# Optimization experiments

Measured on AMD Instinct MI355X. Metric: run time of the kernel, lower is better.

The kernel has to match this reference:

```python
import jax, jax.numpy as jnp
import numpy as np

B, N, D = 16, 4096, 64
LB_TH = 0.01
L2_LAMDA = 0.001
RECONS_LAMDA = 0.2


def _xavier(key, shape):
    fan_in, fan_out = shape[0], shape[1]
    a = float(np.sqrt(6.0 / (fan_in + fan_out)))
    return jax.random.uniform(key, shape, jnp.float32, -a, a)


def setup_inputs() -> dict:
    key = jax.random.key(0)
    k1, k2, k3 = jax.random.split(key, 3)
    X = jax.random.normal(k1, (B, N, D), jnp.float32)
    r_proj = _xavier(k2, (D, D))
    incidence_m = _xavier(k3, (N, N - 1))
    return {"X": X, "r_proj": r_proj, "incidence_m": incidence_m}


def reference(X, r_proj, incidence_m):
    n = incidence_m.shape[0]
    # clamp(min=lb_th) followed by masked_fill(~(v > lb_th), 0) == keep only orig > lb_th
    w = jnp.where(incidence_m > LB_TH, incidence_m, jnp.zeros((), X.dtype))  # [N, N-1]
    # scatter each row's N-1 weights into an NxN matrix, skipping the diagonal
    rows = jnp.arange(n)[:, None]                      # [N,1]
    cols = jnp.arange(n - 1)[None, :]                  # [1,N-1]
    full_cols = cols + (cols >= rows).astype(cols.dtype)  # [N,N-1]
    W = jnp.zeros((n, n), X.dtype).at[rows, full_cols].set(w)
    # per-node projection of master node features: X @ r_proj
    X_proj = jnp.einsum('bnd,de->bne', X, r_proj)      # [B,N,D]
    # neighbor reconstruction for every node at once
    recon = jnp.einsum('ij,bjd->bid', W, X)            # [B,N,D]
    recon_err = jnp.sqrt(jnp.sum((X_proj - recon) ** 2, axis=-1))  # [B,N]
    l1 = jnp.max(jnp.abs(w), axis=1)                   # [N] (max over single-row sum == max abs)
    l2 = jnp.sqrt(jnp.sum(w ** 2, axis=1))             # [N]
    recon_loss = recon_err * RECONS_LAMDA + l1[None, :] + L2_LAMDA * l2[None, :]
    incidence_all = W + jnp.eye(n, dtype=X.dtype)
    return recon_loss, incidence_all
```

## Files before the change

### kernel.cpp

```cpp
#include <hip/hip_runtime.h>
#include <hip/hip_bf16.h>

#define BB 16
#define NN 4096
#define DD 64
#define NM1 4095

typedef __bf16 bf16x8 __attribute__((ext_vector_type(8)));
typedef float f32x4 __attribute__((ext_vector_type(4)));

typedef __attribute__((address_space(1))) const void gas_void;
typedef __attribute__((address_space(3))) void las_void;


__global__ __launch_bounds__(256) void build_kernel(
    const float* __restrict__ inc, float* __restrict__ out_inc,
    __bf16* __restrict__ A16, float* __restrict__ mxa, float* __restrict__ ssa)
{
    int t = threadIdx.x;
    int base = blockIdx.x << 12;
    int rA = (int)((unsigned)base / NM1);
    float pm0 = 0.f, ps0 = 0.f, pm1 = 0.f, ps1 = 0.f;
    #pragma unroll
    for (int j = 0; j < 16; ++j) {
        int f = base + j * 256 + t;
        int i = (int)((unsigned)f / NM1);
        int c = f - i * NM1;
        float x = inc[f];
        float w = x > 0.01f ? x : 0.f;
        int dst = f + i + (c >= i);
        out_inc[dst] = w;
        A16[dst] = (__bf16)w;
        if (i == rA) { pm0 = fmaxf(pm0, w); ps0 += w * w; }
        else         { pm1 = fmaxf(pm1, w); ps1 += w * w; }
    }
    #pragma unroll
    for (int off = 32; off; off >>= 1) {
        pm0 = fmaxf(pm0, __shfl_down(pm0, off));
        ps0 += __shfl_down(ps0, off);
        pm1 = fmaxf(pm1, __shfl_down(pm1, off));
        ps1 += __shfl_down(ps1, off);
    }
    __shared__ float sm0[4], sq0[4], sm1[4], sq1[4];
    int wid = t >> 6;
    if ((t & 63) == 0) { sm0[wid] = pm0; sq0[wid] = ps0; sm1[wid] = pm1; sq1[wid] = ps1; }
    __syncthreads();
    if (t == 0) {
        float m0v = fmaxf(fmaxf(sm0[0], sm0[1]), fmaxf(sm0[2], sm0[3]));
        float s0v = sq0[0] + sq0[1] + sq0[2] + sq0[3];
        float m1v = fmaxf(fmaxf(sm1[0], sm1[1]), fmaxf(sm1[2], sm1[3]));
        float s1v = sq1[0] + sq1[1] + sq1[2] + sq1[3];
        atomicMax((unsigned*)(mxa + rA), __float_as_uint(m0v));
        atomicAdd(ssa + rA, s0v);
        int rB = rA + 1;
        if (rB < NN) {
            atomicMax((unsigned*)(mxa + rB), __float_as_uint(m1v));
            atomicAdd(ssa + rB, s1v);
        }
    }
}

__global__ __launch_bounds__(256) void xt_kernel(
    const float* __restrict__ X, __bf16* __restrict__ XT,
    float* __restrict__ out_inc, __bf16* __restrict__ A16)
{
    __shared__ __bf16 tile[64 * 72];
    int t = threadIdx.x;
    int ntile = blockIdx.x, b = blockIdx.y;
    int n = t >> 2, q = t & 3;
    const float* src = X + ((size_t)b * NN + ntile * 64 + n) * DD + q * 16;
    #pragma unroll
    for (int v = 0; v < 4; ++v) {
        f32x4 u = *(const f32x4*)(src + v * 4);
        #pragma unroll
        for (int j = 0; j < 4; ++j) {
            int d = q * 16 + v * 4 + j;
            tile[d * 72 + n] = (__bf16)u[j];
        }
    }
    __syncthreads();
    int d = t >> 2;
    __bf16* dst = XT + ((size_t)b * DD + d) * NN + ntile * 64 + q * 16;
    *(bf16x8*)dst       = *(bf16x8*)&tile[d * 72 + q * 16];
    *(bf16x8*)(dst + 8) = *(bf16x8*)&tile[d * 72 + q * 16 + 8];
    if (b == 0 && t < 64) {
        int r = ntile * 64 + t;
        out_inc[(size_t)r * NN + r] = 1.0f;
        A16[(size_t)r * NN + r] = (__bf16)1.0f;
    }
}

__global__ __launch_bounds__(512, 2) void gemm_loss_kernel(
    const __bf16* __restrict__ A16, const __bf16* __restrict__ XT,
    const float* __restrict__ X, const float* __restrict__ rproj,
    const float* __restrict__ mxa, const float* __restrict__ ssa,
    float* __restrict__ loss)
{
    __shared__ __bf16 smem[3 * 16384];

    const int t = threadIdx.x;
    const int wave = t >> 6, lane = t & 63;
    const int quad = lane >> 4, ln = lane & 15;
    const int sr = lane >> 3, so = lane & 7;
    const int bq = wave >> 2;
    const int wr = (wave & 3) << 5;
    const int m0 = blockIdx.x * 128;
    const int b0 = blockIdx.y * 2;

    const __bf16* Abase = A16 + (size_t)m0 * NN;
    const __bf16* XTb   = XT + (size_t)b0 * DD * NN;

    f32x4 acc[2][4];
    f32x4 zero = {0.f, 0.f, 0.f, 0.f};
    #pragma unroll
    for (int mt = 0; mt < 2; ++mt)
        #pragma unroll
        for (int ct = 0; ct < 4; ++ct) acc[mt][ct] = zero;

    auto stage = [&](int buf, int kt) {
        __bf16* bA = smem + buf * 16384;
        __bf16* bX = bA + 8192;
        const int k0 = kt << 6;
        #pragma unroll
        for (int p = 0; p < 2; ++p) {
            const int r0 = (p << 6) + (wave << 3);
            const int r  = r0 + sr;
            const int og = so ^ (r & 7);
            __builtin_amdgcn_global_load_lds(
                (gas_void*)(Abase + (size_t)r * NN + k0 + (og << 3)),
                (las_void*)(bA + r0 * 64), 16, 0, 0);
            __builtin_amdgcn_global_load_lds(
                (gas_void*)(XTb + (size_t)r * NN + k0 + (og << 3)),
                (las_void*)(bX + r0 * 64), 16, 0, 0);
        }
    };

    auto compute = [&](int buf) {
        const __bf16* bA = smem + buf * 16384;
        const __bf16* bX = bA + 8192 + (bq << 12);
        #pragma unroll
        for (int kk = 0; kk < 64; kk += 32) {
            const int oc = (kk >> 3) + quad;
            bf16x8 af[2], bfr[4];
            #pragma unroll
            for (int mt = 0; mt < 2; ++mt) {
                const int r = wr + mt * 16 + ln;
                af[mt] = *(const bf16x8*)&bA[r * 64 + ((oc ^ (r & 7)) << 3)];
            }
            #pragma unroll
            for (int ct = 0; ct < 4; ++ct) {
                const int n = ct * 16 + ln;
                bfr[ct] = *(const bf16x8*)&bX[n * 64 + ((oc ^ (n & 7)) << 3)];
            }
            #pragma unroll
            for (int mt = 0; mt < 2; ++mt)
                #pragma unroll
                for (int ct = 0; ct < 4; ++ct)
                    acc[mt][ct] = __builtin_amdgcn_mfma_f32_16x16x32_bf16(
                        af[mt], bfr[ct], acc[mt][ct], 0, 0, 0);
        }
    };

    const int NT = NN / 64;
    stage(0, 0);
    stage(1, 1);
    for (int kt = 0; kt < NT; ++kt) {
        const int nx = kt + 2;
        if (nx < NT) {
            stage(nx % 3, nx);
            asm volatile("s_waitcnt vmcnt(8)" ::: "memory");
        } else if (kt == NT - 2) {
            asm volatile("s_waitcnt vmcnt(4)" ::: "memory");
        } else {
            asm volatile("s_waitcnt vmcnt(0)" ::: "memory");
        }
        __builtin_amdgcn_s_barrier();
        compute(kt % 3);
        asm volatile("" ::: "memory");
        __builtin_amdgcn_s_barrier();
    }

    {
        const int rr = t >> 2, q = t & 3;
        #pragma unroll
        for (int bb = 0; bb < 2; ++bb) {
            const float* xs = X + ((size_t)(b0 + bb) * NN + m0 + rr) * DD + q * 16;
            __bf16* XA = smem + bb * 8192;
            #pragma unroll
            for (int v = 0; v < 2; ++v) {
                f32x4 u0 = *(const f32x4*)(xs + v * 8);
                f32x4 u1 = *(const f32x4*)(xs + v * 8 + 4);
                bf16x8 w;
                #pragma unroll
                for (int j = 0; j < 4; ++j) { w[j] = (__bf16)u0[j]; w[j + 4] = (__bf16)u1[j]; }
                const int o = (q * 2 + v) ^ (rr & 7);
                *(bf16x8*)&XA[rr * 64 + o * 8] = w;
            }
        }
        if (t < 256) {
            const int rr2 = t >> 2, q2 = t & 3;
            const float* rs = rproj + (size_t)rr2 * DD + q2 * 16;
            __bf16* R = smem + 16384;
            #pragma unroll
            for (int v = 0; v < 4; ++v) {
                f32x4 u = *(const f32x4*)(rs + v * 4);
                #pragma unroll
                for (int j = 0; j < 4; ++j) {
                    const int d = q2 * 16 + v * 4 + j;
                    float val = u[j] + (d == rr2 ? 1.0f : 0.0f);
                    R[d * 64 + (((rr2 >> 3) ^ (d & 7)) << 3) + (rr2 & 7)] = (__bf16)val;
                }
            }
        }
    }
    __syncthreads();

    f32x4 dif[2][4];
    #pragma unroll
    for (int mt = 0; mt < 2; ++mt)
        #pragma unroll
        for (int ct = 0; ct < 4; ++ct) dif[mt][ct] = -acc[mt][ct];

    {
        const __bf16* XA = smem + bq * 8192;
        const __bf16* R  = smem + 16384;
        #pragma unroll
        for (int kk = 0; kk < DD; kk += 32) {
            const int oc = (kk >> 3) + quad;
            bf16x8 af[2], bfr[4];
            #pragma unroll
            for (int mt = 0; mt < 2; ++mt) {
                const int r = wr + mt * 16 + ln;
                af[mt] = *(const bf16x8*)&XA[r * 64 + ((oc ^ (r & 7)) << 3)];
            }
            #pragma unroll
            for (int ct = 0; ct < 4; ++ct) {
                const int n = ct * 16 + ln;
                bfr[ct] = *(const bf16x8*)&R[n * 64 + ((oc ^ (n & 7)) << 3)];
            }
            #pragma unroll
            for (int mt = 0; mt < 2; ++mt)
                #pragma unroll
                for (int ct = 0; ct < 4; ++ct)
                    dif[mt][ct] = __builtin_amdgcn_mfma_f32_16x16x32_bf16(
                        af[mt], bfr[ct], dif[mt][ct], 0, 0, 0);
        }
    }

    #pragma unroll
    for (int mt = 0; mt < 2; ++mt) {
        #pragma unroll
        for (int rg = 0; rg < 4; ++rg) {
            float s = 0.f;
            #pragma unroll
            for (int ct = 0; ct < 4; ++ct) {
                float d = dif[mt][ct][rg];
                s += d * d;
            }
            s += __shfl_xor(s, 1);
            s += __shfl_xor(s, 2);
            s += __shfl_xor(s, 4);
            s += __shfl_xor(s, 8);
            if (ln == 0) {
                int row = m0 + wr + mt * 16 + quad * 4 + rg;
                loss[(size_t)(b0 + bq) * NN + row] =
                    0.2f * sqrtf(s) + mxa[row] + 0.001f * sqrtf(ssa[row]);
            }
        }
    }
}

extern "C" void kernel_launch(void* const* d_in, const int* in_sizes, int n_in,
                              void* d_out, int out_size, void* d_ws, size_t ws_size,
                              hipStream_t stream) {
    const float* X   = (const float*)d_in[0];
    const float* r   = (const float*)d_in[1];
    const float* inc = (const float*)d_in[2];
    float* out      = (float*)d_out;
    float* out_loss = out;
    float* out_inc  = out + (size_t)BB * NN;

    char* ws = (char*)d_ws;
    float*  mxa = (float*)ws;
    float*  ssa = (float*)(ws + 16384);
    __bf16* XT  = (__bf16*)(ws + 32768);
    __bf16* A16 = (__bf16*)(ws + 32768 + (size_t)8 * 1024 * 1024);

    hipMemsetAsync(mxa, 0, 32768, stream);

    hipLaunchKernelGGL(build_kernel, dim3(NM1), dim3(256), 0, stream,
                       inc, out_inc, A16, mxa, ssa);
    hipLaunchKernelGGL(xt_kernel, dim3(NN / 64, BB), dim3(256), 0, stream,
                       X, XT, out_inc, A16);
    hipLaunchKernelGGL(gemm_loss_kernel, dim3(NN / 128, BB / 2), dim3(512), 0, stream,
                       A16, XT, X, r, mxa, ssa, out_loss);
}
```

Measured before the change: 190.8 us.

## Load A fragments directly into registers and deepen X pipeline to four stages

The A operand no longer goes through LDS. Each wave loads its own A rows straight into registers with inline-asm global_load_dwordx4, prefetching two steps ahead. Only the XT tile is staged in LDS, now as a 4-buffer ring with a smaller footprint, and the loop is fully unrolled with precomputed pointers and sched barriers. This cuts LDS traffic and address arithmetic, at the cost of more VGPRs for the register-held fragments and uncoalesced per-lane global loads for A.

```diff
diff --git a/kernel.cpp b/kernel.cpp
--- a/kernel.cpp
+++ b/kernel.cpp
@@ -96,7 +96,7 @@
     const float* __restrict__ mxa, const float* __restrict__ ssa,
     float* __restrict__ loss)
 {
-    __shared__ __bf16 smem[3 * 16384];
+    __shared__ __bf16 smem[4 * 8192];
 
     const int t = threadIdx.x;
     const int wave = t >> 6, lane = t & 63;
@@ -107,8 +107,15 @@
     const int m0 = blockIdx.x * 128;
     const int b0 = blockIdx.y * 2;
 
-    const __bf16* Abase = A16 + (size_t)m0 * NN;
-    const __bf16* XTb   = XT + (size_t)b0 * DD * NN;
+    const __bf16* XTb = XT + (size_t)b0 * DD * NN;
+
+    const int rp0 = (wave << 3) + sr;
+    const int og  = so ^ sr;
+    const __bf16* srcB0 = XTb + (size_t)rp0 * NN + og * 8;
+    const __bf16* srcB1 = XTb + (size_t)(rp0 + 64) * NN + og * 8;
+
+    const __bf16* aA0 = A16 + (size_t)(m0 + wr + ln) * NN + quad * 8;
+    const __bf16* aA1 = aA0 + (size_t)16 * NN;
 
     f32x4 acc[2][4];
     f32x4 zero = {0.f, 0.f, 0.f, 0.f};
@@ -117,68 +124,75 @@
         #pragma unroll
         for (int ct = 0; ct < 4; ++ct) acc[mt][ct] = zero;
 
-    auto stage = [&](int buf, int kt) {
-        __bf16* bA = smem + buf * 16384;
-        __bf16* bX = bA + 8192;
-        const int k0 = kt << 6;
-        #pragma unroll
-        for (int p = 0; p < 2; ++p) {
-            const int r0 = (p << 6) + (wave << 3);
-            const int r  = r0 + sr;
-            const int og = so ^ (r & 7);
-            __builtin_amdgcn_global_load_lds(
-                (gas_void*)(Abase + (size_t)r * NN + k0 + (og << 3)),
-                (las_void*)(bA + r0 * 64), 16, 0, 0);
-            __builtin_amdgcn_global_load_lds(
-                (gas_void*)(XTb + (size_t)r * NN + k0 + (og << 3)),
-                (las_void*)(bX + r0 * 64), 16, 0, 0);
-        }
-    };
-
-    auto compute = [&](int buf) {
-        const __bf16* bA = smem + buf * 16384;
-        const __bf16* bX = bA + 8192 + (bq << 12);
-        #pragma unroll
-        for (int kk = 0; kk < 64; kk += 32) {
-            const int oc = (kk >> 3) + quad;
-            bf16x8 af[2], bfr[4];
-            #pragma unroll
-            for (int mt = 0; mt < 2; ++mt) {
-                const int r = wr + mt * 16 + ln;
-                af[mt] = *(const bf16x8*)&bA[r * 64 + ((oc ^ (r & 7)) << 3)];
-            }
-            #pragma unroll
-            for (int ct = 0; ct < 4; ++ct) {
-                const int n = ct * 16 + ln;
-                bfr[ct] = *(const bf16x8*)&bX[n * 64 + ((oc ^ (n & 7)) << 3)];
-            }
-            #pragma unroll
-            for (int mt = 0; mt < 2; ++mt)
-                #pragma unroll
-                for (int ct = 0; ct < 4; ++ct)
-                    acc[mt][ct] = __builtin_amdgcn_mfma_f32_16x16x32_bf16(
-                        af[mt], bfr[ct], acc[mt][ct], 0, 0, 0);
-        }
-    };
-
-    const int NT = NN / 64;
-    stage(0, 0);
-    stage(1, 1);
-    for (int kt = 0; kt < NT; ++kt) {
-        const int nx = kt + 2;
-        if (nx < NT) {
-            stage(nx % 3, nx);
-            asm volatile("s_waitcnt vmcnt(8)" ::: "memory");
-        } else if (kt == NT - 2) {
-            asm volatile("s_waitcnt vmcnt(4)" ::: "memory");
-        } else {
-            asm volatile("s_waitcnt vmcnt(0)" ::: "memory");
-        }
-        __builtin_amdgcn_s_barrier();
-        compute(kt % 3);
-        asm volatile("" ::: "memory");
-        __builtin_amdgcn_s_barrier();
-    }
+    bf16x8 afr[4][2][2];
+
+#define STAGE(BUF) do {                                                        \
+    __builtin_amdgcn_global_load_lds((gas_void*)srcB0,                         \
+        (las_void*)(smem + (BUF) * 8192 + (wave << 3) * 64), 16, 0, 0);        \
+    __builtin_amdgcn_global_load_lds((gas_void*)srcB1,                         \
+        (las_void*)(smem + (BUF) * 8192 + (64 + (wave << 3)) * 64), 16, 0, 0); \
+    srcB0 += 64; srcB1 += 64; } while (0)
+
+#define LOADA(S) do {                                                          \
+    asm volatile("global_load_dwordx4 %0, %2, off\n\t"                         \
+                 "global_load_dwordx4 %1, %2, off offset:64"                   \
+                 : "=&v"(afr[S][0][0]), "=&v"(afr[S][0][1]) : "v"(aA0));       \
+    asm volatile("global_load_dwordx4 %0, %2, off\n\t"                         \
+                 "global_load_dwordx4 %1, %2, off offset:64"                   \
+                 : "=&v"(afr[S][1][0]), "=&v"(afr[S][1][1]) : "v"(aA1));       \
+    aA0 += 64; aA1 += 64; } while (0)
+
+#define VMCNT(N) asm volatile("s_waitcnt vmcnt(" #N ")" ::: "memory")
+
+#define COMPUTE(S) do {                                                        \
+    const __bf16* bX_ = smem + (S) * 8192 + (bq << 12);                        \
+    _Pragma("unroll")                                                          \
+    for (int h = 0; h < 2; ++h) {                                              \
+        const int oc = (h << 2) + quad;                                        \
+        bf16x8 bfr[4];                                                         \
+        _Pragma("unroll")                                                      \
+        for (int ct = 0; ct < 4; ++ct) {                                       \
+            const int n = ct * 16 + ln;                                        \
+            bfr[ct] = *(const bf16x8*)&bX_[n * 64 + ((oc ^ (n & 7)) << 3)];    \
+        }                                                                      \
+        _Pragma("unroll")                                                      \
+        for (int ct = 0; ct < 4; ++ct) {                                       \
+            acc[0][ct] = __builtin_amdgcn_mfma_f32_16x16x32_bf16(              \
+                afr[S][0][h], bfr[ct], acc[0][ct], 0, 0, 0);                   \
+            acc[1][ct] = __builtin_amdgcn_mfma_f32_16x16x32_bf16(              \
+                afr[S][1][h], bfr[ct], acc[1][ct], 0, 0, 0);                   \
+        }                                                                      \
+    } } while (0)
+
+#define STEP(S, T2, STG, VMN) do {                                             \
+    if (STG) { STAGE(T2); LOADA(T2); }                                         \
+    VMCNT(VMN);                                                                \
+    __builtin_amdgcn_sched_barrier(0);                                         \
+    __builtin_amdgcn_s_barrier();                                              \
+    __builtin_amdgcn_sched_barrier(0);                                         \
+    COMPUTE(S); } while (0)
+
+    STAGE(0); LOADA(0);
+    STAGE(1); LOADA(1);
+
+    for (int g = 0; g < 15; ++g) {
+        STEP(0, 2, true, 12);
+        STEP(1, 3, true, 12);
+        STEP(2, 0, true, 12);
+        STEP(3, 1, true, 12);
+    }
+    STEP(0, 2, true, 12);
+    STEP(1, 3, true, 12);
+    STEP(2, 0, false, 6);
+    STEP(3, 0, false, 0);
+
+#undef STEP
+#undef COMPUTE
+#undef VMCNT
+#undef LOADA
+#undef STAGE
+
+    __syncthreads();
 
     {
         const int rr = t >> 2, q = t & 3;
@@ -215,11 +229,10 @@
     }
     __syncthreads();
 
-    f32x4 dif[2][4];
     #pragma unroll
     for (int mt = 0; mt < 2; ++mt)
         #pragma unroll
-        for (int ct = 0; ct < 4; ++ct) dif[mt][ct] = -acc[mt][ct];
+        for (int ct = 0; ct < 4; ++ct) acc[mt][ct] = -acc[mt][ct];
 
     {
         const __bf16* XA = smem + bq * 8192;
@@ -242,8 +255,8 @@
             for (int mt = 0; mt < 2; ++mt)
                 #pragma unroll
                 for (int ct = 0; ct < 4; ++ct)
-                    dif[mt][ct] = __builtin_amdgcn_mfma_f32_16x16x32_bf16(
-                        af[mt], bfr[ct], dif[mt][ct], 0, 0, 0);
+                    acc[mt][ct] = __builtin_amdgcn_mfma_f32_16x16x32_bf16(
+                        af[mt], bfr[ct], acc[mt][ct], 0, 0, 0);
         }
     }
 
@@ -254,7 +267,7 @@
             float s = 0.f;
             #pragma unroll
             for (int ct = 0; ct < 4; ++ct) {
-                float d = dif[mt][ct][rg];
+                float d = acc[mt][ct][rg];
                 s += d * d;
             }
             s += __shfl_xor(s, 1);
```

After: 218.3 us. 1.14x slower.

## Use 4-stage LDS pipeline with one barrier per K-step and MFMA priority

Applied to the files above, without the earlier changes.

Grows the shared-memory ring from 3 to 4 buffers and restructures the main GEMM loop. Each K-step now waits once, barriers once, computes, then issues the next stage's async global-to-LDS loads into the buffer freed by the previous step. This removes the second barrier per iteration, and the last three steps are peeled into an explicit tail. The MFMA section also raises wave priority with s_setprio and adds sched_barrier fences to keep loads and compute from being reordered. The cost is 128KB of LDS per block instead of 96KB, which should not change residency since two blocks already did not fit. It also relies on precise vmcnt accounting for correctness.

```diff
diff --git a/kernel.cpp b/kernel.cpp
--- a/kernel.cpp
+++ b/kernel.cpp
@@ -96,7 +96,7 @@
     const float* __restrict__ mxa, const float* __restrict__ ssa,
     float* __restrict__ loss)
 {
-    __shared__ __bf16 smem[3 * 16384];
+    __shared__ __bf16 smem[4 * 16384];
 
     const int t = threadIdx.x;
     const int wave = t >> 6, lane = t & 63;
@@ -138,6 +138,7 @@
     auto compute = [&](int buf) {
         const __bf16* bA = smem + buf * 16384;
         const __bf16* bX = bA + 8192 + (bq << 12);
+        __builtin_amdgcn_s_setprio(1);
         #pragma unroll
         for (int kk = 0; kk < 64; kk += 32) {
             const int oc = (kk >> 3) + quad;
@@ -159,26 +160,34 @@
                     acc[mt][ct] = __builtin_amdgcn_mfma_f32_16x16x32_bf16(
                         af[mt], bfr[ct], acc[mt][ct], 0, 0, 0);
         }
+        __builtin_amdgcn_s_setprio(0);
     };
 
     const int NT = NN / 64;
     stage(0, 0);
     stage(1, 1);
-    for (int kt = 0; kt < NT; ++kt) {
-        const int nx = kt + 2;
-        if (nx < NT) {
-            stage(nx % 3, nx);
-            asm volatile("s_waitcnt vmcnt(8)" ::: "memory");
-        } else if (kt == NT - 2) {
-            asm volatile("s_waitcnt vmcnt(4)" ::: "memory");
-        } else {
-            asm volatile("s_waitcnt vmcnt(0)" ::: "memory");
-        }
+    stage(2, 2);
+    for (int kt = 0; kt < NT - 3; ++kt) {
+        asm volatile("s_waitcnt vmcnt(8)" ::: "memory");
         __builtin_amdgcn_s_barrier();
-        compute(kt % 3);
-        asm volatile("" ::: "memory");
-        __builtin_amdgcn_s_barrier();
-    }
+        __builtin_amdgcn_sched_barrier(0);
+        compute(kt & 3);
+        stage((kt + 3) & 3, kt + 3);
+    }
+    asm volatile("s_waitcnt vmcnt(8)" ::: "memory");
+    __builtin_amdgcn_s_barrier();
+    __builtin_amdgcn_sched_barrier(0);
+    compute(1);
+    asm volatile("s_waitcnt vmcnt(4)" ::: "memory");
+    __builtin_amdgcn_s_barrier();
+    __builtin_amdgcn_sched_barrier(0);
+    compute(2);
+    asm volatile("s_waitcnt vmcnt(0)" ::: "memory");
+    __builtin_amdgcn_s_barrier();
+    __builtin_amdgcn_sched_barrier(0);
+    compute(3);
+
+    __syncthreads();
 
     {
         const int rr = t >> 2, q = t & 3;
@@ -215,11 +224,10 @@
     }
     __syncthreads();
 
-    f32x4 dif[2][4];
     #pragma unroll
     for (int mt = 0; mt < 2; ++mt)
         #pragma unroll
-        for (int ct = 0; ct < 4; ++ct) dif[mt][ct] = -acc[mt][ct];
+        for (int ct = 0; ct < 4; ++ct) acc[mt][ct] = -acc[mt][ct];
 
     {
         const __bf16* XA = smem + bq * 8192;
@@ -242,8 +250,8 @@
             for (int mt = 0; mt < 2; ++mt)
                 #pragma unroll
                 for (int ct = 0; ct < 4; ++ct)
-                    dif[mt][ct] = __builtin_amdgcn_mfma_f32_16x16x32_bf16(
-                        af[mt], bfr[ct], dif[mt][ct], 0, 0, 0);
+                    acc[mt][ct] = __builtin_amdgcn_mfma_f32_16x16x32_bf16(
+                        af[mt], bfr[ct], acc[mt][ct], 0, 0, 0);
         }
     }
 
@@ -254,7 +262,7 @@
             float s = 0.f;
             #pragma unroll
             for (int ct = 0; ct < 4; ++ct) {
-                float d = dif[mt][ct][rg];
+                float d = acc[mt][ct][rg];
                 s += d * d;
             }
             s += __shfl_xor(s, 1);
```

After: 185.5 us (median of 2 runs). 2.8% less time.
